# Kernel optimization log

Hardware: AMD Instinct MI355X
Metric: run time of the kernel (lower is better)

The kernel has to match this reference:

```python
import jax, jax.numpy as jnp
import numpy as np

EPS = 1e-5

def layer_norm(x, w, b):
    m = jnp.mean(x, axis=-1, keepdims=True)
    v = jnp.mean(jnp.square(x - m), axis=-1, keepdims=True)
    return (x - m) * jax.lax.rsqrt(v + EPS) * w + b

def setup_inputs() -> dict:
    key = jax.random.key(0)
    B, S, D, H = 4, 2048, 768, 12
    Dh, F = D // H, 4 * D
    ks = jax.random.split(key, 16)
    s = 0.02
    return {
        "x":    jax.random.normal(ks[0], (B, S, D), dtype=jnp.float32),
        # per-head q/k/v projections stacked over heads: [H, D, Dh]
        "Wq":   jax.random.normal(ks[1], (H, D, Dh), dtype=jnp.float32) * s,
        "bq":   jnp.zeros((H, Dh), dtype=jnp.float32),
        "Wk":   jax.random.normal(ks[2], (H, D, Dh), dtype=jnp.float32) * s,
        "bk":   jnp.zeros((H, Dh), dtype=jnp.float32),
        "Wv":   jax.random.normal(ks[3], (H, D, Dh), dtype=jnp.float32) * s,
        "bv":   jnp.zeros((H, Dh), dtype=jnp.float32),
        "Wo":   jax.random.normal(ks[4], (D, D), dtype=jnp.float32) * s,
        "bo":   jnp.zeros((D,), dtype=jnp.float32),
        "W1":   jax.random.normal(ks[5], (D, F), dtype=jnp.float32) * s,
        "b1":   jnp.zeros((F,), dtype=jnp.float32),
        "W2":   jax.random.normal(ks[6], (F, D), dtype=jnp.float32) * s,
        "b2":   jnp.zeros((D,), dtype=jnp.float32),
        "ln1_w": jnp.ones((D,), dtype=jnp.float32),
        "ln1_b": jnp.zeros((D,), dtype=jnp.float32),
        "ln2_w": jnp.ones((D,), dtype=jnp.float32),
        "ln2_b": jnp.zeros((D,), dtype=jnp.float32),
    }

def reference(x, Wq, bq, Wk, bk, Wv, bv, Wo, bo, W1, b1, W2, b2,
              ln1_w, ln1_b, ln2_w, ln2_b):
    B, S, D = x.shape
    H, _, Dh = Wq.shape
    scale = jnp.sqrt(jnp.float32(Dh))  # torch scales by sqrt(dout)
    # q,k,v: [B, H, S, Dh]
    q = jnp.einsum('bsd,hde->bhse', x, Wq) + bq[None, :, None, :]
    k = jnp.einsum('bsd,hde->bhse', x, Wk) + bk[None, :, None, :]
    v = jnp.einsum('bsd,hde->bhse', x, Wv) + bv[None, :, None, :]
    scores = jnp.einsum('bhqe,bhke->bhqk', q, k) / scale  # [B,H,S,S]
    causal = jnp.tril(jnp.ones((S, S), dtype=bool))
    scores = jnp.where(causal[None, None], scores, -jnp.inf)
    attn = jax.nn.softmax(scores, axis=-1)
    ctx = jnp.einsum('bhqk,bhke->bhqe', attn, v)           # [B,H,S,Dh]
    ctx = jnp.transpose(ctx, (0, 2, 1, 3)).reshape(B, S, D)  # concat heads
    att_out = ctx @ Wo + bo
    h = layer_norm(x + att_out, ln1_w, ln1_b)  # post-norm, dropout=0
    ff = jax.nn.gelu(h @ W1 + b1, approximate=False) @ W2 + b2
    return layer_norm(h + ff, ln2_w, ln2_b)
```

## Files before the change

### kernel.cpp

```cpp
#include <hip/hip_runtime.h>
#include <hip/hip_bf16.h>
#include <math.h>

#define B_ 4
#define S_ 2048
#define D_ 768
#define H_ 12
#define DH_ 64
#define F_ 3072
#define NTOK (B_*S_)
#define BH_ (B_*H_)

typedef __hip_bfloat16 bf16;
typedef __attribute__((ext_vector_type(8))) short bf16x8;
typedef __attribute__((ext_vector_type(4))) float f32x4;
typedef __attribute__((ext_vector_type(4))) _Float16 half4;
typedef __attribute__((ext_vector_type(8))) _Float16 half8;
typedef __attribute__((ext_vector_type(2))) __fp16 fp16x2;

#define GLD16(g, l) __builtin_amdgcn_global_load_lds( \
    (__attribute__((address_space(1))) void*)(uintptr_t)(g), \
    (__attribute__((address_space(3))) void*)(uintptr_t)(l), 16, 0, 0)

__device__ __forceinline__ float bs2f(short s){
  union { unsigned int u; float f; } cv; cv.u = ((unsigned int)(unsigned short)s) << 16; return cv.f;
}
__device__ __forceinline__ float b2f(bf16 v){ return __bfloat162float(v); }
__device__ __forceinline__ bf16 f2b(float v){ return __float2bfloat16(v); }
__device__ __forceinline__ short f2bb(float v){ bf16 b = f2b(v); short s; __builtin_memcpy(&s, &b, 2); return s; }

__device__ __forceinline__ half4 pk4(float p0, float p1, float p2, float p3){
  union { fp16x2 v2[2]; half4 v4; } u;
  u.v2[0] = __builtin_amdgcn_cvt_pkrtz(p0, p1);
  u.v2[1] = __builtin_amdgcn_cvt_pkrtz(p2, p3);
  return u.v4;
}

__device__ __forceinline__ void wgbar(){
  __builtin_amdgcn_s_barrier();
  asm volatile("" ::: "memory");
}
__device__ __forceinline__ void wgbar_lds(){
  asm volatile("s_waitcnt lgkmcnt(0)" ::: "memory");
  __builtin_amdgcn_s_barrier();
  asm volatile("" ::: "memory");
}

__device__ __forceinline__ float gelu_fast(float v){
  const float c0 = -2.302208157f;
  const float c1 = -0.102943238f;
  float w = v*v;
  float z = v * __builtin_fmaf(c1, w, c0);
  float t = __builtin_amdgcn_exp2f(z);
  return v * __builtin_amdgcn_rcpf(1.0f + t);
}

__global__ __launch_bounds__(256) void prep_k(
    const float4* __restrict__ x4, short4* __restrict__ xb4,
    const float* __restrict__ Wo, bf16* __restrict__ WoT,
    const float* __restrict__ W1, bf16* __restrict__ W1T,
    const float* __restrict__ W2, bf16* __restrict__ W2T,
    const float* __restrict__ Wq, const float* __restrict__ bq,
    const float* __restrict__ Wk, const float* __restrict__ bk,
    const float* __restrict__ Wv, const float* __restrict__ bv,
    bf16* __restrict__ Wt, float* __restrict__ bcat)
{
  __shared__ float t[32][33];
  int bid = blockIdx.x;
  const int tidx = threadIdx.x;

  if (bid < 6144){
    const int i = bid*256 + tidx;
    float4 v = x4[i];
    short4 o;
    o.x = f2bb(v.x); o.y = f2bb(v.y); o.z = f2bb(v.z); o.w = f2bb(v.w);
    xb4[i] = o;
    return;
  }
  bid -= 6144;
  if (bid >= 576 + 2304 + 2304){
    bid -= 576 + 2304 + 2304;
    const int idx = bid*256 + tidx;
    {
      int n = idx / D_;
      int k = idx - n*D_;
      int which = n / D_;
      int cc = n - which*D_;
      int h = cc >> 6, e = cc & 63;
      const float* W = (which==0) ? Wq : ((which==1) ? Wk : Wv);
      Wt[idx] = f2b(W[((size_t)h*D_ + k)*DH_ + e]);
    }
    if (idx < 3*D_){
      int which = idx / D_;
      int cc = idx - which*D_;
      int h = cc >> 6, e = cc & 63;
      const float* bb = (which==0) ? bq : ((which==1) ? bk : bv);
      bcat[idx] = bb[h*DH_ + e];
    }
    return;
  }
  const float* tin; bf16* tout; int K, N, tiles_x;
  if (bid < 576){ tin = Wo; tout = WoT; K = D_; N = D_; tiles_x = 24; }
  else if (bid < 576 + 2304){ bid -= 576; tin = W1; tout = W1T; K = D_; N = F_; tiles_x = 96; }
  else { bid -= 576 + 2304; tin = W2; tout = W2T; K = F_; N = D_; tiles_x = 24; }
  const int kb = (bid / tiles_x)*32, nb = (bid % tiles_x)*32;
  const int xx = tidx & 31, y = tidx >> 5;
#pragma unroll
  for (int yy = y; yy < 32; yy += 8)
    t[yy][xx] = tin[(size_t)(kb+yy)*N + nb + xx];
  __syncthreads();
#pragma unroll
  for (int yy = y; yy < 32; yy += 8)
    tout[(size_t)(nb+yy)*K + kb + xx] = f2b(t[xx][yy]);
}

template<int EPI>
__global__ __launch_bounds__(256) void mgemm128_k(
    const bf16* __restrict__ A, const bf16* __restrict__ Bt,
    const float* __restrict__ bias, const bf16* __restrict__ aux,
    bf16* __restrict__ C, int M, int N, int K,
    bf16* __restrict__ qb, bf16* __restrict__ kbuf, _Float16* __restrict__ vt)
{
  __shared__ __align__(16) bf16 As[16384];
  __shared__ __align__(16) bf16 Bs[16384];
  const int tid  = threadIdx.x;
  const int wave = tid >> 6, lane = tid & 63;
  const int quad = lane >> 4, l16 = lane & 15;
  const int wm = (wave >> 1) * 64, wn = (wave & 1) * 64;

  const int NX = gridDim.x;
  const int f  = blockIdx.y * NX + blockIdx.x;
  const int xcd = f & 7;
  const int j   = f >> 3;
  const int bx  = j % NX;
  const int by  = (j / NX) * 8 + xcd;
  const int m0 = by * 128, n0 = bx * 128;

  const int srow8 = lane >> 3;
  const int g     = (lane & 7) ^ srow8;
  const bf16* gA = A  + (size_t)(m0 + wave*32 + srow8)*K + g*8;
  const bf16* gB = Bt + (size_t)(n0 + wave*32 + srow8)*K + g*8;
  const uintptr_t asb = (uintptr_t)(void*)As + (size_t)wave*32*128;
  const uintptr_t bsb = (uintptr_t)(void*)Bs + (size_t)wave*32*128;

  f32x4 acc[4][4];
#pragma unroll
  for (int i=0;i<4;i++)
#pragma unroll
    for (int j2=0;j2<4;j2++) acc[i][j2] = (f32x4)0.f;

  const char* AsB = (const char*)As;
  const char* BsB = (const char*)Bs;
  const int KT = K >> 6;

#pragma unroll
  for (int t=0;t<4;t++){
    GLD16(gA + (size_t)t*8*K, asb + t*1024);
    GLD16(gB + (size_t)t*8*K, bsb + t*1024);
  }
  gA += 64; gB += 64;
  asm volatile("s_waitcnt vmcnt(0)" ::: "memory");
  wgbar();

  for (int kt = 0; kt < KT; ++kt){
    const int cur = kt & 1, nxt = cur ^ 1;
    const bool pf = (kt + 1) < KT;
    if (pf){
      const uintptr_t ao = asb + (size_t)nxt*16384;
      const uintptr_t bo = bsb + (size_t)nxt*16384;
#pragma unroll
      for (int t=0;t<4;t++){
        GLD16(gA + (size_t)t*8*K, ao + t*1024);
        GLD16(gB + (size_t)t*8*K, bo + t*1024);
      }
      gA += 64; gB += 64;
    }
    const char* Ac = AsB + (size_t)cur*16384;
    const char* Bc = BsB + (size_t)cur*16384;
#pragma unroll
    for (int kq = 0; kq < 2; kq++){
      const int cbase = kq*4 + quad;
      bf16x8 af[4], bfr[4];
#pragma unroll
      for (int i=0;i<4;i++){
        const int m = wm + i*16 + l16;
        af[i] = *(const bf16x8*)(Ac + (m << 7) + ((cbase ^ (m & 7)) << 4));
      }
#pragma unroll
      for (int j2=0;j2<4;j2++){
        const int n = wn + j2*16 + l16;
        bfr[j2] = *(const bf16x8*)(Bc + (n << 7) + ((cbase ^ (n & 7)) << 4));
      }
#pragma unroll
      for (int i=0;i<4;i++)
#pragma unroll
        for (int j2=0;j2<4;j2++)
          acc[i][j2] = __builtin_amdgcn_mfma_f32_16x16x32_bf16(af[i], bfr[j2], acc[i][j2], 0, 0, 0);
    }
    if (pf) asm volatile("s_waitcnt vmcnt(0)" ::: "memory");
    wgbar();
  }

#pragma unroll
  for (int i=0;i<4;i++){
#pragma unroll
    for (int j2=0;j2<4;j2++){
      const int n = n0 + wn + j2*16 + l16;
      const int m_base = m0 + wm + i*16 + quad*4;
      if (EPI == 0){
        const int which = n / D_;
        const int cc = n - which*D_;
        const int h = cc >> 6, e = cc & 63;
        if (which == 2){
          const int b = m_base >> 11, s = m_base & (S_-1);
          const int sl = s & 63;
          const int perm = (sl & 32) | (((sl >> 2) & 3) << 3) | ((sl & 16) >> 2);
          half4 hv;
#pragma unroll
          for (int r=0;r<4;r++) hv[r] = (_Float16)(acc[i][j2][r] + bias[n]);
          *(half4*)(vt + ((size_t)(b*H_+h)*DH_ + e)*S_ + (s & ~63) + perm) = hv;
        } else {
          bf16* dst = (which==0) ? qb : kbuf;
          const float sc2 = (which==0) ? 0.18033688f : 1.0f;
#pragma unroll
          for (int r=0;r<4;r++){
            const int m = m_base + r;
            const int b = m >> 11, s = m & (S_-1);
            dst[((size_t)(b*H_+h)*S_ + s)*DH_ + e] = f2b((acc[i][j2][r] + bias[n]) * sc2);
          }
        }
      } else if (EPI == 1){
#pragma unroll
        for (int r=0;r<4;r++){
          const int m = m_base + r;
          float v = acc[i][j2][r] + bias[n] + b2f(aux[(size_t)m*N + n]);
          C[(size_t)m*N + n] = f2b(v);
        }
      } else {
#pragma unroll
        for (int r=0;r<4;r++){
          const int m = m_base + r;
          float v = acc[i][j2][r] + bias[n];
          C[(size_t)m*N + n] = f2b(gelu_fast(v));
        }
      }
    }
  }
}

__global__ __launch_bounds__(256) void mgemmN64_k(
    const bf16* __restrict__ A, const bf16* __restrict__ Bt,
    const float* __restrict__ bias, const bf16* __restrict__ aux,
    bf16* __restrict__ C, int M, int N, int K)
{
  __shared__ __align__(16) bf16 As[16384];
  __shared__ __align__(16) bf16 Bs[8192];
  const int tid  = threadIdx.x;
  const int wave = tid >> 6, lane = tid & 63;
  const int quad = lane >> 4, l16 = lane & 15;
  const int wm = (wave >> 1) * 64, wn = (wave & 1) * 32;

  const int NX = gridDim.x;
  const int f  = blockIdx.y * NX + blockIdx.x;
  const int xcd = f & 7;
  const int j   = f >> 3;
  const int bx  = j % NX;
  const int by  = (j / NX) * 8 + xcd;
  const int m0 = by * 128, n0 = bx * 64;

  const int srow8 = lane >> 3;
  const int g     = (lane & 7) ^ srow8;
  const bf16* gA = A  + (size_t)(m0 + wave*32 + srow8)*K + g*8;
  const bf16* gB = Bt + (size_t)(n0 + wave*16 + srow8)*K + g*8;
  const uintptr_t asb = (uintptr_t)(void*)As + (size_t)wave*32*128;
  const uintptr_t bsb = (uintptr_t)(void*)Bs + (size_t)wave*16*128;

  f32x4 acc[4][2];
#pragma unroll
  for (int i=0;i<4;i++)
#pragma unroll
    for (int j2=0;j2<2;j2++) acc[i][j2] = (f32x4)0.f;

  const char* AsB = (const char*)As;
  const char* BsB = (const char*)Bs;
  const int KT = K >> 6;

#pragma unroll
  for (int t=0;t<4;t++) GLD16(gA + (size_t)t*8*K, asb + t*1024);
#pragma unroll
  for (int t=0;t<2;t++) GLD16(gB + (size_t)t*8*K, bsb + t*1024);
  gA += 64; gB += 64;
  asm volatile("s_waitcnt vmcnt(0)" ::: "memory");
  wgbar();

  for (int kt = 0; kt < KT; ++kt){
    const int cur = kt & 1, nxt = cur ^ 1;
    const bool pf = (kt + 1) < KT;
    if (pf){
      const uintptr_t ao = asb + (size_t)nxt*16384;
      const uintptr_t bo = bsb + (size_t)nxt*8192;
#pragma unroll
      for (int t=0;t<4;t++) GLD16(gA + (size_t)t*8*K, ao + t*1024);
#pragma unroll
      for (int t=0;t<2;t++) GLD16(gB + (size_t)t*8*K, bo + t*1024);
      gA += 64; gB += 64;
    }
    const char* Ac = AsB + (size_t)cur*16384;
    const char* Bc = BsB + (size_t)cur*8192;
#pragma unroll
    for (int kq = 0; kq < 2; kq++){
      const int cbase = kq*4 + quad;
      bf16x8 af[4], bfr[2];
#pragma unroll
      for (int i=0;i<4;i++){
        const int m = wm + i*16 + l16;
        af[i] = *(const bf16x8*)(Ac + (m << 7) + ((cbase ^ (m & 7)) << 4));
      }
#pragma unroll
      for (int j2=0;j2<2;j2++){
        const int n = wn + j2*16 + l16;
        bfr[j2] = *(const bf16x8*)(Bc + (n << 7) + ((cbase ^ (n & 7)) << 4));
      }
#pragma unroll
      for (int i=0;i<4;i++)
#pragma unroll
        for (int j2=0;j2<2;j2++)
          acc[i][j2] = __builtin_amdgcn_mfma_f32_16x16x32_bf16(af[i], bfr[j2], acc[i][j2], 0, 0, 0);
    }
    if (pf) asm volatile("s_waitcnt vmcnt(0)" ::: "memory");
    wgbar();
  }

#pragma unroll
  for (int i=0;i<4;i++){
#pragma unroll
    for (int j2=0;j2<2;j2++){
      const int n = n0 + wn + j2*16 + l16;
      const int m_base = m0 + wm + i*16 + quad*4;
#pragma unroll
      for (int r=0;r<4;r++){
        const int m = m_base + r;
        float v = acc[i][j2][r] + bias[n] + b2f(aux[(size_t)m*N + n]);
        C[(size_t)m*N + n] = f2b(v);
      }
    }
  }
}

__global__ __launch_bounds__(256, 4) void fattn_k(const bf16* __restrict__ qb,
    const bf16* __restrict__ kb, const _Float16* __restrict__ vt, bf16* __restrict__ ctx)
{
  __shared__ __align__(16) char smem[32768];
  char* kp0 = smem;
  char* kp1 = smem + 8192;
  char* vp0 = smem + 16384;
  char* vp1 = smem + 24576;

  const int bh = blockIdx.x;
  const int qt = 31 - blockIdx.y;
  const int q0 = qt * 64;
  const int tid = threadIdx.x;
  const int wave = tid >> 6, lane = tid & 63;
  const int quad = lane >> 4, l16 = lane & 15;
  const size_t kbase = (size_t)bh * S_ * DH_;
  const int nt = qt + 1;

  const int sr = tid >> 2;
  const int c0 = (tid & 3) * 2;
  const int w0 = sr*128 + ((c0 ^ (sr & 7)) << 4);
  const int w1 = sr*128 + (((c0 + 1) ^ (sr & 7)) << 4);
  const int ge0 = c0*8, ge1 = c0*8 + 8;

  const int sA0 = ((quad       ^ (l16 & 7)) << 4);
  const int sA1 = (((4 + quad) ^ (l16 & 7)) << 4);

  const int qloc = wave*16 + l16;
  const int qglob = q0 + qloc;
  bf16x8 qf[2];
#pragma unroll
  for (int h=0; h<2; h++)
    qf[h] = *(const bf16x8*)(qb + kbase + (size_t)qglob*DH_ + h*32 + quad*8);

  f32x4 o[4];
#pragma unroll
  for (int df=0; df<4; df++) o[df] = (f32x4)0.f;
  float mi = -1e30f, li = 0.f;

  bf16x8 ka0, ka1; half8 va0, va1;
  {
    const bf16* ks = kb + kbase + (size_t)sr*DH_;
    ka0 = *(const bf16x8*)(ks + ge0);
    ka1 = *(const bf16x8*)(ks + ge1);
    const _Float16* vs = vt + ((size_t)bh*DH_ + sr)*S_;
    va0 = *(const half8*)(vs + ge0);
    va1 = *(const half8*)(vs + ge1);
  }
  *(bf16x8*)(kp0 + w0) = ka0;
  *(bf16x8*)(kp0 + w1) = ka1;
  *(half8*)(vp0 + w0)  = va0;
  *(half8*)(vp0 + w1)  = va1;
  if (nt > 1){
    const bf16* ks = kb + kbase + (size_t)(64 + sr)*DH_;
    ka0 = *(const bf16x8*)(ks + ge0);
    ka1 = *(const bf16x8*)(ks + ge1);
    const _Float16* vs = vt + ((size_t)bh*DH_ + sr)*S_ + 64;
    va0 = *(const half8*)(vs + ge0);
    va1 = *(const half8*)(vs + ge1);
  }
  wgbar_lds();

  for (int kt = 0; kt < nt; ++kt){
    f32x4 sc[4];
#pragma unroll
    for (int mf=0; mf<4; mf++){
      const int rb = (mf*16 + l16) * 128;
      bf16x8 a0 = *(const bf16x8*)(kp0 + rb + sA0);
      bf16x8 a1 = *(const bf16x8*)(kp0 + rb + sA1);
      f32x4 t = __builtin_amdgcn_mfma_f32_16x16x32_bf16(a0, qf[0], (f32x4)0.f, 0, 0, 0);
      sc[mf]  = __builtin_amdgcn_mfma_f32_16x16x32_bf16(a1, qf[1], t, 0, 0, 0);
    }

    if (kt == qt){
#pragma unroll
      for (int mf=0; mf<4; mf++){
        const int keyl = mf*16 + quad*4;
#pragma unroll
        for (int r=0; r<4; r++)
          if (keyl + r > qloc) sc[mf][r] = -1e30f;
      }
    }

    float mx = -1e30f;
#pragma unroll
    for (int mf=0; mf<4; mf++)
#pragma unroll
      for (int r=0; r<4; r++) mx = fmaxf(mx, sc[mf][r]);
    mx = fmaxf(mx, __shfl_xor(mx, 16));
    mx = fmaxf(mx, __shfl_xor(mx, 32));

    half8 vva[4], vvb[4];
#pragma unroll
    for (int df=0; df<4; df++){
      const int rb = (df*16 + l16) * 128;
      vva[df] = *(const half8*)(vp0 + rb + sA0);
      vvb[df] = *(const half8*)(vp0 + rb + sA1);
    }

    if (kt + 1 < nt){
      *(bf16x8*)(kp1 + w0) = ka0;
      *(bf16x8*)(kp1 + w1) = ka1;
      *(half8*)(vp1 + w0)  = va0;
      *(half8*)(vp1 + w1)  = va1;
      if (kt + 2 < nt){
        const int k0n = (kt + 2) * 64;
        const bf16* ks = kb + kbase + (size_t)(k0n + sr)*DH_;
        ka0 = *(const bf16x8*)(ks + ge0);
        ka1 = *(const bf16x8*)(ks + ge1);
        const _Float16* vs = vt + ((size_t)bh*DH_ + sr)*S_ + k0n;
        va0 = *(const half8*)(vs + ge0);
        va1 = *(const half8*)(vs + ge1);
      }
    }
    wgbar_lds();

    const bool need = !__all(mx - mi <= 8.f);
    if (need){
      const float mn = fmaxf(mi, mx);
      const float a = __builtin_amdgcn_exp2f(mi - mn);
      mi = mn; li *= a;
#pragma unroll
      for (int df=0; df<4; df++)
#pragma unroll
        for (int r=0; r<4; r++) o[df][r] *= a;
    }

    half4 pfr[4];
    float rs = 0.f;
#pragma unroll
    for (int mf=0; mf<4; mf++){
      const float p0 = __builtin_amdgcn_exp2f(sc[mf][0] - mi);
      const float p1 = __builtin_amdgcn_exp2f(sc[mf][1] - mi);
      const float p2 = __builtin_amdgcn_exp2f(sc[mf][2] - mi);
      const float p3 = __builtin_amdgcn_exp2f(sc[mf][3] - mi);
      rs += (p0 + p1) + (p2 + p3);
      pfr[mf] = pk4(p0, p1, p2, p3);
    }
    rs += __shfl_xor(rs, 16);
    rs += __shfl_xor(rs, 32);
    li += rs;

    half8 p01 = __builtin_shufflevector(pfr[0], pfr[1], 0,1,2,3,4,5,6,7);
    half8 p23 = __builtin_shufflevector(pfr[2], pfr[3], 0,1,2,3,4,5,6,7);
#pragma unroll
    for (int df=0; df<4; df++){
      o[df] = __builtin_amdgcn_mfma_f32_16x16x32_f16(vva[df], p01, o[df], 0, 0, 0);
      o[df] = __builtin_amdgcn_mfma_f32_16x16x32_f16(vvb[df], p23, o[df], 0, 0, 0);
    }

    { char* t_ = kp0; kp0 = kp1; kp1 = t_; }
    { char* t_ = vp0; vp0 = vp1; vp1 = t_; }
  }

  const int b = bh / H_, h = bh - (bh / H_)*H_;
  const float inv = 1.0f / li;
  short* cdst = (short*)ctx + ((size_t)(b*S_ + qglob))*D_ + h*DH_;
#pragma unroll
  for (int df=0; df<4; df++){
    short4 pk;
    pk.x = f2bb(o[df][0] * inv);
    pk.y = f2bb(o[df][1] * inv);
    pk.z = f2bb(o[df][2] * inv);
    pk.w = f2bb(o[df][3] * inv);
    *(short4*)(cdst + df*16 + quad*4) = pk;
  }
}

template<typename T> __device__ __forceinline__ void st4(T* p, size_t idx, float a, float b, float c, float d);
template<> __device__ __forceinline__ void st4<float>(float* p, size_t idx, float a, float b, float c, float d){
  float4 v; v.x=a; v.y=b; v.z=c; v.w=d; *(float4*)(p+idx) = v;
}
template<> __device__ __forceinline__ void st4<bf16>(bf16* p, size_t idx, float a, float b, float c, float d){
  short4 v; v.x=f2bb(a); v.y=f2bb(b); v.z=f2bb(c); v.w=f2bb(d); *(short4*)((short*)p+idx) = v;
}

template<typename OutT>
__global__ __launch_bounds__(192) void layernorm_k(const bf16* __restrict__ X,
    const float* __restrict__ g, const float* __restrict__ bta, OutT* __restrict__ Y)
{
  const int row = blockIdx.x;
  const int tid = threadIdx.x;
  const short4 raw = *(const short4*)((const short*)X + (size_t)row*D_ + tid*4);
  const float v0 = bs2f(raw.x), v1 = bs2f(raw.y), v2 = bs2f(raw.z), v3 = bs2f(raw.w);
  float s  = v0+v1+v2+v3;
  float s2 = v0*v0+v1*v1+v2*v2+v3*v3;
#pragma unroll
  for (int o = 32; o > 0; o >>= 1){ s += __shfl_down(s, o); s2 += __shfl_down(s2, o); }
  __shared__ float rs[3], rq[3];
  const int lane = tid & 63, w = tid >> 6;
  if (lane == 0){ rs[w] = s; rq[w] = s2; }
  __syncthreads();
  s  = rs[0]+rs[1]+rs[2];
  s2 = rq[0]+rq[1]+rq[2];
  const float mean = s * (1.0f/D_);
  const float var  = s2 * (1.0f/D_) - mean*mean;
  const float inv  = rsqrtf(var + 1e-5f);
  const float4 g4 = *(const float4*)(g + tid*4);
  const float4 b4 = *(const float4*)(bta + tid*4);
  st4(Y, (size_t)row*D_ + tid*4,
      (v0-mean)*inv*g4.x + b4.x,
      (v1-mean)*inv*g4.y + b4.y,
      (v2-mean)*inv*g4.z + b4.z,
      (v3-mean)*inv*g4.w + b4.w);
}

extern "C" void kernel_launch(void* const* d_in, const int* in_sizes, int n_in,
                              void* d_out, int out_size, void* d_ws, size_t ws_size,
                              hipStream_t stream)
{
  const float* x   = (const float*)d_in[0];
  const float* Wq  = (const float*)d_in[1];
  const float* bq  = (const float*)d_in[2];
  const float* Wk  = (const float*)d_in[3];
  const float* bk  = (const float*)d_in[4];
  const float* Wv  = (const float*)d_in[5];
  const float* bv  = (const float*)d_in[6];
  const float* Wo  = (const float*)d_in[7];
  const float* bo  = (const float*)d_in[8];
  const float* W1  = (const float*)d_in[9];
  const float* b1  = (const float*)d_in[10];
  const float* W2  = (const float*)d_in[11];
  const float* b2  = (const float*)d_in[12];
  const float* g1  = (const float*)d_in[13];
  const float* be1 = (const float*)d_in[14];
  const float* g2  = (const float*)d_in[15];
  const float* be2 = (const float*)d_in[16];
  float* out = (float*)d_out;

  char* ws = (char*)d_ws;
  size_t off = 0;
  auto alloc = [&](size_t bytes)->char*{
    char* p = ws + off; off = (off + bytes + 255) & ~(size_t)255; return p;
  };
  bf16*  xb    = (bf16*) alloc((size_t)NTOK*D_*2);
  bf16*  WcatT = (bf16*) alloc((size_t)3*D_*D_*2);
  float* bcat  = (float*)alloc((size_t)3*D_*4);
  bf16*  WoT   = (bf16*) alloc((size_t)D_*D_*2);
  bf16*  W1T   = (bf16*) alloc((size_t)F_*D_*2);
  bf16*  W2T   = (bf16*) alloc((size_t)D_*F_*2);
  bf16*  r1    = (bf16*) alloc((size_t)NTOK*F_*2);
  bf16*  qb    = r1;
  bf16*  kb    = r1 + (size_t)NTOK*D_;
  _Float16* vt = (_Float16*)(r1 + (size_t)2*NTOK*D_);
  bf16*  ff1   = r1;
  bf16*  ctxb  = (bf16*) alloc((size_t)NTOK*D_*2);
  bf16*  y1    = (bf16*) alloc((size_t)NTOK*D_*2);
  bf16*  hb    = (bf16*) alloc((size_t)NTOK*D_*2);
  bf16*  y2    = ctxb;

  prep_k<<<18240, 256, 0, stream>>>(
      (const float4*)x, (short4*)xb, Wo, WoT, W1, W1T, W2, W2T,
      Wq, bq, Wk, bk, Wv, bv, WcatT, bcat);

  mgemm128_k<0><<<dim3(3*D_/128, NTOK/128), 256, 0, stream>>>(
      xb, WcatT, bcat, nullptr, nullptr, NTOK, 3*D_, D_, qb, kb, vt);

  fattn_k<<<dim3(BH_, S_/64), 256, 0, stream>>>(qb, kb, vt, ctxb);

  mgemmN64_k<<<dim3(D_/64, NTOK/128), 256, 0, stream>>>(
      ctxb, WoT, bo, xb, y1, NTOK, D_, D_);

  layernorm_k<bf16><<<NTOK, 192, 0, stream>>>(y1, g1, be1, hb);

  mgemm128_k<2><<<dim3(F_/128, NTOK/128), 256, 0, stream>>>(
      hb, W1T, b1, nullptr, ff1, NTOK, F_, D_, nullptr, nullptr, nullptr);

  mgemmN64_k<<<dim3(D_/64, NTOK/128), 256, 0, stream>>>(
      ff1, W2T, b2, hb, y2, NTOK, D_, F_);

  layernorm_k<float><<<NTOK, 192, 0, stream>>>(y2, g2, be2, out);
}
```

Measured before the change: 346.1 us.

## Halve GEMM K-tile to 32 with new swizzled LDS layout for higher occupancy

The 128x128 bf16 GEMM drops its K step from 64 to 32, halving the double-buffered LDS for A and B from 64KB to 32KB. Global-to-LDS loads and the XOR-swizzled addressing are reworked so two 64-row halves share one 128-byte row. The goal is to fit more workgroups per CU and overlap better. In exchange it runs twice as many loop iterations with a barrier and vmcnt wait each, and less MFMA work per sync.

Result: no change. 350.5 us (+1.3%).

```diff
diff --git a/kernel.cpp b/kernel.cpp
--- a/kernel.cpp
+++ b/kernel.cpp
@@ -121,8 +121,8 @@
     bf16* __restrict__ C, int M, int N, int K,
     bf16* __restrict__ qb, bf16* __restrict__ kbuf, _Float16* __restrict__ vt)
 {
-  __shared__ __align__(16) bf16 As[16384];
-  __shared__ __align__(16) bf16 Bs[16384];
+  __shared__ __align__(16) bf16 As[8192];
+  __shared__ __align__(16) bf16 Bs[8192];
   const int tid  = threadIdx.x;
   const int wave = tid >> 6, lane = tid & 63;
   const int quad = lane >> 4, l16 = lane & 15;
@@ -136,12 +136,22 @@
   const int by  = (j / NX) * 8 + xcd;
   const int m0 = by * 128, n0 = bx * 128;
 
-  const int srow8 = lane >> 3;
-  const int g     = (lane & 7) ^ srow8;
-  const bf16* gA = A  + (size_t)(m0 + wave*32 + srow8)*K + g*8;
-  const bf16* gB = Bt + (size_t)(n0 + wave*32 + srow8)*K + g*8;
-  const uintptr_t asb = (uintptr_t)(void*)As + (size_t)wave*32*128;
-  const uintptr_t bsb = (uintptr_t)(void*)Bs + (size_t)wave*32*128;
+  const int rr1 = tid >> 3, sl = tid & 7;
+  const int rr2 = rr1 + 32;
+  const int gc1 = sl ^ (rr1 & 7);
+  const int gc2 = sl ^ (rr2 & 7);
+  const int sm1 = rr1 + 64*(gc1 >> 2), sk1 = (gc1 & 3)*8;
+  const int sm2 = rr2 + 64*(gc2 >> 2), sk2 = (gc2 & 3)*8;
+  const bf16* gA1 = A  + (size_t)(m0 + sm1)*K + sk1;
+  const bf16* gA2 = A  + (size_t)(m0 + sm2)*K + sk2;
+  const bf16* gB1 = Bt + (size_t)(n0 + sm1)*K + sk1;
+  const bf16* gB2 = Bt + (size_t)(n0 + sm2)*K + sk2;
+  const uintptr_t asb = (uintptr_t)(void*)As + (size_t)wave*1024;
+  const uintptr_t bsb = (uintptr_t)(void*)Bs + (size_t)wave*1024;
+
+  const int hA = wm >> 6, hB = wn >> 6;
+  const int scA = ((hA*4 + quad) ^ (l16 & 7)) << 4;
+  const int scB = ((hB*4 + quad) ^ (l16 & 7)) << 4;
 
   f32x4 acc[4][4];
 #pragma unroll
@@ -151,14 +161,11 @@
 
   const char* AsB = (const char*)As;
   const char* BsB = (const char*)Bs;
-  const int KT = K >> 6;
-
-#pragma unroll
-  for (int t=0;t<4;t++){
-    GLD16(gA + (size_t)t*8*K, asb + t*1024);
-    GLD16(gB + (size_t)t*8*K, bsb + t*1024);
-  }
-  gA += 64; gB += 64;
+  const int KT = K >> 5;
+
+  GLD16(gA1, asb);        GLD16(gA2, asb + 4096);
+  GLD16(gB1, bsb);        GLD16(gB2, bsb + 4096);
+  gA1 += 32; gA2 += 32; gB1 += 32; gB2 += 32;
   asm volatile("s_waitcnt vmcnt(0)" ::: "memory");
   wgbar();
 
@@ -166,37 +173,24 @@
     const int cur = kt & 1, nxt = cur ^ 1;
     const bool pf = (kt + 1) < KT;
     if (pf){
-      const uintptr_t ao = asb + (size_t)nxt*16384;
-      const uintptr_t bo = bsb + (size_t)nxt*16384;
-#pragma unroll
-      for (int t=0;t<4;t++){
-        GLD16(gA + (size_t)t*8*K, ao + t*1024);
-        GLD16(gB + (size_t)t*8*K, bo + t*1024);
-      }
-      gA += 64; gB += 64;
-    }
-    const char* Ac = AsB + (size_t)cur*16384;
-    const char* Bc = BsB + (size_t)cur*16384;
-#pragma unroll
-    for (int kq = 0; kq < 2; kq++){
-      const int cbase = kq*4 + quad;
-      bf16x8 af[4], bfr[4];
-#pragma unroll
-      for (int i=0;i<4;i++){
-        const int m = wm + i*16 + l16;
-        af[i] = *(const bf16x8*)(Ac + (m << 7) + ((cbase ^ (m & 7)) << 4));
-      }
-#pragma unroll
-      for (int j2=0;j2<4;j2++){
-        const int n = wn + j2*16 + l16;
-        bfr[j2] = *(const bf16x8*)(Bc + (n << 7) + ((cbase ^ (n & 7)) << 4));
-      }
-#pragma unroll
-      for (int i=0;i<4;i++)
-#pragma unroll
-        for (int j2=0;j2<4;j2++)
-          acc[i][j2] = __builtin_amdgcn_mfma_f32_16x16x32_bf16(af[i], bfr[j2], acc[i][j2], 0, 0, 0);
-    }
+      GLD16(gA1, asb + nxt*8192);        GLD16(gA2, asb + nxt*8192 + 4096);
+      GLD16(gB1, bsb + nxt*8192);        GLD16(gB2, bsb + nxt*8192 + 4096);
+      gA1 += 32; gA2 += 32; gB1 += 32; gB2 += 32;
+    }
+    const char* Ac = AsB + cur*8192;
+    const char* Bc = BsB + cur*8192;
+    bf16x8 af[4], bfr[4];
+#pragma unroll
+    for (int i=0;i<4;i++)
+      af[i] = *(const bf16x8*)(Ac + ((i*16 + l16) << 7) + scA);
+#pragma unroll
+    for (int j2=0;j2<4;j2++)
+      bfr[j2] = *(const bf16x8*)(Bc + ((j2*16 + l16) << 7) + scB);
+#pragma unroll
+    for (int i=0;i<4;i++)
+#pragma unroll
+      for (int j2=0;j2<4;j2++)
+        acc[i][j2] = __builtin_amdgcn_mfma_f32_16x16x32_bf16(af[i], bfr[j2], acc[i][j2], 0, 0, 0);
     if (pf) asm volatile("s_waitcnt vmcnt(0)" ::: "memory");
     wgbar();
   }
@@ -213,8 +207,8 @@
         const int h = cc >> 6, e = cc & 63;
         if (which == 2){
           const int b = m_base >> 11, s = m_base & (S_-1);
-          const int sl = s & 63;
-          const int perm = (sl & 32) | (((sl >> 2) & 3) << 3) | ((sl & 16) >> 2);
+          const int sl2 = s & 63;
+          const int perm = (sl2 & 32) | (((sl2 >> 2) & 3) << 3) | ((sl2 & 16) >> 2);
           half4 hv;
 #pragma unroll
           for (int r=0;r<4;r++) hv[r] = (_Float16)(acc[i][j2][r] + bias[n]);
```
